# Kernel tuning notes

Measured on AMD Instinct MI355X. Metric: run time of the kernel, lower is better.

## Reference

```python
import jax, jax.numpy as jnp
import numpy as np

B, S, D, H = 4, 2048, 1024, 16
DK = D // H

def setup_inputs() -> dict:
    key = jax.random.key(0)
    ks = jax.random.split(key, 8)
    Q = jax.random.normal(ks[0], (B, S, D), dtype=jnp.float32)
    K = jax.random.normal(ks[1], (B, S, D), dtype=jnp.float32)
    V = jax.random.normal(ks[2], (B, S, D), dtype=jnp.float32)
    # causal mask: 0 means masked (as in masked_fill(mask == 0, -inf))
    mask = jnp.broadcast_to(jnp.tril(jnp.ones((S, S), dtype=jnp.int32))[None, None], (B, 1, S, S))
    scale = 1.0 / np.sqrt(D)
    W_Q = jax.random.normal(ks[3], (D, D), dtype=jnp.float32) * scale
    W_K = jax.random.normal(ks[4], (D, D), dtype=jnp.float32) * scale
    W_V = jax.random.normal(ks[5], (D, D), dtype=jnp.float32) * scale
    W_O = jax.random.normal(ks[6], (D, D), dtype=jnp.float32) * scale
    return {"Q": Q, "K": K, "V": V, "mask": mask,
            "W_Q": W_Q, "W_K": W_K, "W_V": W_V, "W_O": W_O}

def _split_heads(x):
    # [B, S, D] -> [B, H, S, DK]
    b, s, _ = x.shape
    return x.reshape(b, s, H, DK).transpose(0, 2, 1, 3)

def reference(Q, K, V, mask, W_Q, W_K, W_V, W_O):
    # nn.Linear(d,d,bias=False): y = x @ W.T ; here W_* stored as [D, D]
    q = _split_heads(Q @ W_Q.T)
    k = _split_heads(K @ W_K.T)
    v = _split_heads(V @ W_V.T)
    scores = jnp.einsum('bhqd,bhkd->bhqk', q, k) / jnp.sqrt(jnp.float32(DK))
    scores = jnp.where(mask == 0, -jnp.inf, scores)
    weights = jax.nn.softmax(scores, axis=-1)
    weights = jnp.nan_to_num(weights, nan=0.0)  # fully-masked rows -> 0
    # dropout is identity at eval / p=0
    attn = jnp.einsum('bhqk,bhkd->bhqd', weights, v)
    attn = attn.transpose(0, 2, 1, 3).reshape(Q.shape[0], Q.shape[1], D)
    return attn @ W_O.T
```

## Files before the change

### kernel.cpp

```cpp
#include <hip/hip_runtime.h>
#include <stdint.h>

#define B_  4
#define S_  2048
#define D_  1024
#define H_  16
#define DK_ 64

typedef __attribute__((ext_vector_type(8)))  short   short8;
typedef __attribute__((ext_vector_type(8)))  unsigned short ushort8;
typedef __attribute__((ext_vector_type(4)))  float   f32x4;
typedef __attribute__((ext_vector_type(16))) float   f32x16;

#define GPTR(p) ((const __attribute__((address_space(1))) void*)(p))
#define SPTR(p) ((__attribute__((address_space(3))) void*)(p))

__device__ inline unsigned short f2bf(float f) {
  uint32_t u = __float_as_uint(f);
  uint32_t r = (u + 0x7fffu + ((u >> 16) & 1u)) >> 16;
  return (unsigned short)r;
}
__device__ inline float bf2f(unsigned short h) {
  return __uint_as_float(((uint32_t)h) << 16);
}
__device__ inline uint32_t pkbf(float a, float b) {
  uint32_t r;
  asm("v_cvt_pk_bf16_f32 %0, %1, %2" : "=v"(r) : "v"(a), "v"(b));
  return r;
}
__device__ inline void pl32(uint32_t& a, uint32_t& b) {
  asm volatile("v_permlane32_swap_b32 %0, %1" : "+v"(a), "+v"(b));
}
__device__ inline short8 mk8(uint32_t a, uint32_t b, uint32_t c, uint32_t d) {
  union { uint32_t u[4]; short8 s; } x;
  x.u[0] = a; x.u[1] = b; x.u[2] = c; x.u[3] = d;
  return x.s;
}

__global__ __launch_bounds__(256) void conv_one(const float* __restrict__ src,
                                                unsigned short* __restrict__ dst,
                                                size_t n) {
  size_t i = ((size_t)blockIdx.x * blockDim.x + threadIdx.x) * 4;
  if (i < n) {
    float4 v = *reinterpret_cast<const float4*>(src + i);
    ushort4 o;
    o.x = f2bf(v.x); o.y = f2bf(v.y); o.z = f2bf(v.z); o.w = f2bf(v.w);
    *reinterpret_cast<ushort4*>(dst + i) = o;
  }
}

__global__ __launch_bounds__(256) void conv_x3(const float* __restrict__ q,
                                               const float* __restrict__ k,
                                               const float* __restrict__ v,
                                               unsigned short* __restrict__ dst) {
  const size_t NX = (size_t)B_ * S_ * D_;
  const float* src = (blockIdx.z == 0) ? q : (blockIdx.z == 1) ? k : v;
  unsigned short* d = dst + (size_t)blockIdx.z * NX;
  size_t i = ((size_t)blockIdx.x * blockDim.x + threadIdx.x) * 4;
  float4 vv = *reinterpret_cast<const float4*>(src + i);
  ushort4 o;
  o.x = f2bf(vv.x); o.y = f2bf(vv.y); o.z = f2bf(vv.z); o.w = f2bf(vv.w);
  *reinterpret_cast<ushort4*>(d + i) = o;
}

__global__ __launch_bounds__(256) void conv_w4(const float* __restrict__ w0,
                                               const float* __restrict__ w1,
                                               const float* __restrict__ w2,
                                               const float* __restrict__ w3,
                                               unsigned short* __restrict__ dst) {
  const size_t NW = (size_t)D_ * D_;
  const float* src = (blockIdx.z == 0) ? w0 : (blockIdx.z == 1) ? w1
                   : (blockIdx.z == 2) ? w2 : w3;
  unsigned short* d = dst + (size_t)blockIdx.z * NW;
  size_t i = ((size_t)blockIdx.x * blockDim.x + threadIdx.x) * 4;
  if (i < NW) {
    float4 v = *reinterpret_cast<const float4*>(src + i);
    ushort4 o;
    o.x = f2bf(v.x); o.y = f2bf(v.y); o.z = f2bf(v.z); o.w = f2bf(v.w);
    *reinterpret_cast<ushort4*>(d + i) = o;
  }
}

#define BM 128
#define BN 128
#define BK 32

__global__ __launch_bounds__(256) void gemm_qkv(const unsigned short* __restrict__ X0,
                                                const unsigned short* __restrict__ X1,
                                                const unsigned short* __restrict__ X2,
                                                const unsigned short* __restrict__ W,
                                                unsigned short* __restrict__ P,
                                                int zbase) {
  const size_t NW = (size_t)D_ * D_;
  const size_t NX = (size_t)B_ * S_ * D_;
  const int z = zbase + blockIdx.z;

  const unsigned short* A;
  const unsigned short* Bm;
  unsigned short* C;
  int N, m0, n0;
  if (z == 2) {
    A = W + 2 * NW; Bm = X2; C = P + 2 * NX;
    N = B_ * S_;
    m0 = (blockIdx.x >> 6) * BM;
    n0 = (blockIdx.x & 63) * BN;
  } else {
    A = z ? X1 : X0; Bm = W + (size_t)z * NW; C = P + (size_t)z * NX;
    N = D_;
    m0 = (blockIdx.x & 63) * BM;
    n0 = (blockIdx.x >> 6) * BN;
  }
  const int K = D_;

  __shared__ unsigned short sA[3][BM * BK];
  __shared__ unsigned short sB[3][BN * BK];

  const int tid  = threadIdx.x;
  const int lane = tid & 63;
  const int wid  = tid >> 6;
  const int wr   = wid >> 1, wc = wid & 1;
  const int g = lane >> 4, c = lane & 15;

  f32x4 acc[4][4];
#pragma unroll
  for (int m = 0; m < 4; ++m)
#pragma unroll
    for (int n = 0; n < 4; ++n) acc[m][n] = (f32x4){0.f, 0.f, 0.f, 0.f};

  auto stage = [&](int kt_, int bs) {
    const int k0 = kt_ * BK;
#pragma unroll
    for (int i = 0; i < 2; ++i) {
      const int base_ob = i * 4096 + wid * 1024;
      const int ob  = base_ob + lane * 16;
      const int row = ob >> 6;
      const int scb = (ob & 63) ^ (((ob >> 7) & 3) << 4);
      const unsigned short* ga = A  + (size_t)(m0 + row) * K + k0 + (scb >> 1);
      const unsigned short* gb = Bm + (size_t)(n0 + row) * K + k0 + (scb >> 1);
      __builtin_amdgcn_global_load_lds(GPTR(ga), SPTR(&sA[bs][base_ob >> 1]), 16, 0, 0);
      __builtin_amdgcn_global_load_lds(GPTR(gb), SPTR(&sB[bs][base_ob >> 1]), 16, 0, 0);
    }
  };

  const int nkt = K / BK;
  stage(0, 0);
  stage(1, 1);
  for (int kt = 0; kt < nkt; ++kt) {
    const int cur = kt % 3;
    if (kt + 2 < nkt) {
      stage(kt + 2, (kt + 2) % 3);
      asm volatile("s_waitcnt vmcnt(8)" ::: "memory");
    } else if (kt + 1 < nkt) {
      asm volatile("s_waitcnt vmcnt(4)" ::: "memory");
    } else {
      asm volatile("s_waitcnt vmcnt(0)" ::: "memory");
    }
    __builtin_amdgcn_sched_barrier(0);
    __builtin_amdgcn_s_barrier();
    __builtin_amdgcn_sched_barrier(0);

    short8 af[4], bf[4];
#pragma unroll
    for (int m = 0; m < 4; ++m) {
      const int ra = wr * 64 + m * 16 + c;
      af[m] = *reinterpret_cast<const short8*>(
          &sA[cur][ra * BK + ((g ^ ((ra >> 1) & 3)) << 3)]);
    }
#pragma unroll
    for (int n = 0; n < 4; ++n) {
      const int rb = wc * 64 + n * 16 + c;
      bf[n] = *reinterpret_cast<const short8*>(
          &sB[cur][rb * BK + ((g ^ ((rb >> 1) & 3)) << 3)]);
    }
    __builtin_amdgcn_s_setprio(1);
#pragma unroll
    for (int m = 0; m < 4; ++m)
#pragma unroll
      for (int n = 0; n < 4; ++n)
        acc[m][n] = __builtin_amdgcn_mfma_f32_16x16x32_bf16(af[m], bf[n], acc[m][n], 0, 0, 0);
    __builtin_amdgcn_s_setprio(0);

    asm volatile("s_waitcnt lgkmcnt(0)" ::: "memory");
    __builtin_amdgcn_sched_barrier(0);
    __builtin_amdgcn_s_barrier();
    __builtin_amdgcn_sched_barrier(0);
  }

#pragma unroll
  for (int m = 0; m < 4; ++m)
#pragma unroll
    for (int n = 0; n < 4; ++n)
#pragma unroll
      for (int r = 0; r < 4; ++r) {
        const int row = m0 + wr * 64 + m * 16 + 4 * g + r;
        const int col = n0 + wc * 64 + n * 16 + c;
        C[(size_t)row * N + col] = f2bf(acc[m][n][r]);
      }
}

__global__ __launch_bounds__(256) void gemm_out(const unsigned short* __restrict__ A,
                                                const unsigned short* __restrict__ Bm,
                                                float* __restrict__ C,
                                                int M, int N, int K) {
  __shared__ unsigned short sA[3][BM * BK];
  __shared__ unsigned short sB[3][BN * BK];

  const int tid  = threadIdx.x;
  const int lane = tid & 63;
  const int wid  = tid >> 6;
  const int wr   = wid >> 1, wc = wid & 1;
  const int g = lane >> 4, c = lane & 15;

  const int m0 = blockIdx.x * BM;
  const int n0 = blockIdx.y * BN;

  f32x4 acc[4][4];
#pragma unroll
  for (int m = 0; m < 4; ++m)
#pragma unroll
    for (int n = 0; n < 4; ++n) acc[m][n] = (f32x4){0.f, 0.f, 0.f, 0.f};

  auto stage = [&](int kt_, int bs) {
    const int k0 = kt_ * BK;
#pragma unroll
    for (int i = 0; i < 2; ++i) {
      const int base_ob = i * 4096 + wid * 1024;
      const int ob  = base_ob + lane * 16;
      const int row = ob >> 6;
      const int scb = (ob & 63) ^ (((ob >> 7) & 3) << 4);
      const unsigned short* ga = A  + (size_t)(m0 + row) * K + k0 + (scb >> 1);
      const unsigned short* gb = Bm + (size_t)(n0 + row) * K + k0 + (scb >> 1);
      __builtin_amdgcn_global_load_lds(GPTR(ga), SPTR(&sA[bs][base_ob >> 1]), 16, 0, 0);
      __builtin_amdgcn_global_load_lds(GPTR(gb), SPTR(&sB[bs][base_ob >> 1]), 16, 0, 0);
    }
  };

  const int nkt = K / BK;
  stage(0, 0);
  stage(1, 1);
  for (int kt = 0; kt < nkt; ++kt) {
    const int cur = kt % 3;
    if (kt + 2 < nkt) {
      stage(kt + 2, (kt + 2) % 3);
      asm volatile("s_waitcnt vmcnt(8)" ::: "memory");
    } else if (kt + 1 < nkt) {
      asm volatile("s_waitcnt vmcnt(4)" ::: "memory");
    } else {
      asm volatile("s_waitcnt vmcnt(0)" ::: "memory");
    }
    __builtin_amdgcn_sched_barrier(0);
    __builtin_amdgcn_s_barrier();
    __builtin_amdgcn_sched_barrier(0);

    short8 af[4], bf[4];
#pragma unroll
    for (int m = 0; m < 4; ++m) {
      const int ra = wr * 64 + m * 16 + c;
      af[m] = *reinterpret_cast<const short8*>(
          &sA[cur][ra * BK + ((g ^ ((ra >> 1) & 3)) << 3)]);
    }
#pragma unroll
    for (int n = 0; n < 4; ++n) {
      const int rb = wc * 64 + n * 16 + c;
      bf[n] = *reinterpret_cast<const short8*>(
          &sB[cur][rb * BK + ((g ^ ((rb >> 1) & 3)) << 3)]);
    }
    __builtin_amdgcn_s_setprio(1);
#pragma unroll
    for (int m = 0; m < 4; ++m)
#pragma unroll
      for (int n = 0; n < 4; ++n)
        acc[m][n] = __builtin_amdgcn_mfma_f32_16x16x32_bf16(af[m], bf[n], acc[m][n], 0, 0, 0);
    __builtin_amdgcn_s_setprio(0);

    asm volatile("s_waitcnt lgkmcnt(0)" ::: "memory");
    __builtin_amdgcn_sched_barrier(0);
    __builtin_amdgcn_s_barrier();
    __builtin_amdgcn_sched_barrier(0);
  }

#pragma unroll
  for (int m = 0; m < 4; ++m)
#pragma unroll
    for (int n = 0; n < 4; ++n)
#pragma unroll
      for (int r = 0; r < 4; ++r) {
        const int row = m0 + wr * 64 + m * 16 + 4 * g + r;
        const int col = n0 + wc * 64 + n * 16 + c;
        C[(size_t)row * N + col] = acc[m][n][r];
      }
}

__global__ __launch_bounds__(256, 4) void attn_fwd(const unsigned short* __restrict__ qp,
                                                   const unsigned short* __restrict__ kp,
                                                   const unsigned short* __restrict__ vtp,
                                                   unsigned short* __restrict__ attn) {
  const int bh = blockIdx.x;
  const int bx = blockIdx.y;
  const int b = bh >> 4, h = bh & 15;

  __shared__ unsigned short smem[4 * 64 * 64];

  const int tid  = threadIdx.x;
  const int lane = tid & 63;
  const int wid  = tid >> 6;
  const int hi   = lane >> 5;
  const int lo5  = lane & 31;

  const size_t headoff  = (size_t)b * S_ * D_ + (size_t)h * DK_;
  const size_t vheadoff = (size_t)(h * DK_) * (size_t)(B_ * S_) + (size_t)b * S_;

  const int xk = (lo5 & 7) << 4;

  auto stage = [&](int kt_, int bs) {
#pragma unroll
    for (int i = 0; i < 2; ++i) {
      const int base_ob = i * 4096 + wid * 1024;
      const int ob  = base_ob + lane * 16;
      const int row = ob >> 7;
      const int scb = (ob & 127) ^ ((row & 7) << 4);
      const unsigned short* gk = &kp[headoff + (size_t)(kt_ * 64 + row) * D_ + (scb >> 1)];
      const unsigned short* gv = &vtp[vheadoff + (size_t)row * (B_ * S_) + kt_ * 64 + (scb >> 1)];
      __builtin_amdgcn_global_load_lds(GPTR(gk), SPTR(&smem[bs * 4096 + (base_ob >> 1)]), 16, 0, 0);
      __builtin_amdgcn_global_load_lds(GPTR(gv), SPTR(&smem[8192 + bs * 4096 + (base_ob >> 1)]), 16, 0, 0);
    }
  };

#pragma unroll 1
  for (int pass = 0; pass < 2; ++pass) {
    const int qtile = pass ? bx : (15 - bx);
    const int qw = qtile * 128 + wid * 32;
    const int qg = qw + lo5;

    __syncthreads();

    short8 aq[4];
#pragma unroll
    for (int t = 0; t < 4; ++t) {
      ushort8 raw = *reinterpret_cast<const ushort8*>(
          &qp[headoff + (size_t)qg * D_ + t * 16 + hi * 8]);
      short8 sv;
#pragma unroll
      for (int j = 0; j < 8; ++j) sv[j] = (short)f2bf(bf2f(raw[j]) * 0.125f);
      aq[t] = sv;
    }

    float mrun = -3.0e38f, lrun = 0.f;
    f32x16 oa0, oa1;
#pragma unroll
    for (int r = 0; r < 16; ++r) { oa0[r] = 0.f; oa1[r] = 0.f; }

    const int nkv = 2 * (qtile + 1);
    stage(0, 0);

    for (int kt = 0; kt < nkv; ++kt) {
      const int cur = kt & 1;
      if (kt < nkv - 1) {
        stage(kt + 1, cur ^ 1);
        asm volatile("s_waitcnt vmcnt(4)" ::: "memory");
      } else {
        asm volatile("s_waitcnt vmcnt(0)" ::: "memory");
      }
      __builtin_amdgcn_sched_barrier(0);
      __builtin_amdgcn_s_barrier();
      __builtin_amdgcn_sched_barrier(0);

      const int kv0 = kt * 64;
      if (kv0 <= qw + 31) {
        const unsigned short* Kb = &smem[cur * 4096];
        const unsigned short* Vb = &smem[8192 + cur * 4096];

        f32x16 st0, st1;
#pragma unroll
        for (int r = 0; r < 16; ++r) { st0[r] = 0.f; st1[r] = 0.f; }
        __builtin_amdgcn_s_setprio(1);
#pragma unroll
        for (int t = 0; t < 4; ++t) {
          const int off = ((32 * t + 16 * hi) ^ xk) >> 1;
          short8 k0 = *reinterpret_cast<const short8*>(&Kb[lo5 * 64 + off]);
          short8 k1 = *reinterpret_cast<const short8*>(&Kb[(32 + lo5) * 64 + off]);
          st0 = __builtin_amdgcn_mfma_f32_32x32x16_bf16(k0, aq[t], st0, 0, 0, 0);
          st1 = __builtin_amdgcn_mfma_f32_32x32x16_bf16(k1, aq[t], st1, 0, 0, 0);
        }
        __builtin_amdgcn_s_setprio(0);

        if (kv0 + 63 > qw) {
#pragma unroll
          for (int r = 0; r < 16; ++r) {
            const int kvl = kv0 + (r & 3) + 8 * (r >> 2) + 4 * hi;
            if (kvl > qg)      st0[r] = -3.0e38f;
            if (kvl + 32 > qg) st1[r] = -3.0e38f;
          }
        }

        float tm = fmaxf(st0[0], st1[0]);
#pragma unroll
        for (int r = 1; r < 16; ++r) tm = fmaxf(tm, fmaxf(st0[r], st1[r]));
        tm = fmaxf(tm, __shfl_xor(tm, 32));
        const bool grow = !__all(tm <= mrun + 8.0f);
        float alpha = 1.0f;
        if (grow) {
          const float newm = fmaxf(mrun, tm);
          alpha = __expf(mrun - newm);
          mrun = newm;
        }

        float ls = 0.f;
#pragma unroll
        for (int r = 0; r < 16; ++r) { st0[r] = __expf(st0[r] - mrun); ls += st0[r]; }
        uint32_t a0 = pkbf(st0[0],  st0[1]),  a1 = pkbf(st0[2],  st0[3]);
        uint32_t b0 = pkbf(st0[4],  st0[5]),  b1 = pkbf(st0[6],  st0[7]);
        uint32_t c0 = pkbf(st0[8],  st0[9]),  c1 = pkbf(st0[10], st0[11]);
        uint32_t d0 = pkbf(st0[12], st0[13]), d1 = pkbf(st0[14], st0[15]);
        pl32(a0, b0); pl32(a1, b1);
        pl32(c0, d0); pl32(c1, d1);
        short8 pf0 = mk8(a0, a1, b0, b1);
        short8 pf1 = mk8(c0, c1, d0, d1);

#pragma unroll
        for (int r = 0; r < 16; ++r) { st1[r] = __expf(st1[r] - mrun); ls += st1[r]; }
        uint32_t e0 = pkbf(st1[0],  st1[1]),  e1 = pkbf(st1[2],  st1[3]);
        uint32_t f0 = pkbf(st1[4],  st1[5]),  f1 = pkbf(st1[6],  st1[7]);
        uint32_t g0 = pkbf(st1[8],  st1[9]),  g1 = pkbf(st1[10], st1[11]);
        uint32_t h0 = pkbf(st1[12], st1[13]), h1 = pkbf(st1[14], st1[15]);
        pl32(e0, f0); pl32(e1, f1);
        pl32(g0, h0); pl32(g1, h1);
        short8 pf2 = mk8(e0, e1, f0, f1);
        short8 pf3 = mk8(g0, g1, h0, h1);

        ls += __shfl_xor(ls, 32);
        if (grow) {
          lrun = lrun * alpha + ls;
#pragma unroll
          for (int r = 0; r < 16; ++r) { oa0[r] *= alpha; oa1[r] *= alpha; }
        } else {
          lrun += ls;
        }

        __builtin_amdgcn_s_setprio(1);
#pragma unroll
        for (int c4 = 0; c4 < 4; ++c4) {
          const int off = ((32 * c4 + 16 * hi) ^ xk) >> 1;
          short8 v0 = *reinterpret_cast<const short8*>(&Vb[lo5 * 64 + off]);
          short8 v1 = *reinterpret_cast<const short8*>(&Vb[(32 + lo5) * 64 + off]);
          const short8 pf = (c4 == 0) ? pf0 : (c4 == 1) ? pf1 : (c4 == 2) ? pf2 : pf3;
          oa0 = __builtin_amdgcn_mfma_f32_32x32x16_bf16(v0, pf, oa0, 0, 0, 0);
          oa1 = __builtin_amdgcn_mfma_f32_32x32x16_bf16(v1, pf, oa1, 0, 0, 0);
        }
        __builtin_amdgcn_s_setprio(0);
      }

      asm volatile("s_waitcnt lgkmcnt(0)" ::: "memory");
      __builtin_amdgcn_sched_barrier(0);
      __builtin_amdgcn_s_barrier();
      __builtin_amdgcn_sched_barrier(0);
    }

    {
      unsigned short* sO = &smem[wid * (32 * 72)];
      const float inv = 1.0f / lrun;
#pragma unroll
      for (int r = 0; r < 16; ++r) {
        const int dl = (r & 3) + 8 * (r >> 2) + 4 * hi;
        sO[lo5 * 72 + dl]      = f2bf(oa0[r] * inv);
        sO[lo5 * 72 + 32 + dl] = f2bf(oa1[r] * inv);
      }
      asm volatile("s_waitcnt lgkmcnt(0)" ::: "memory");
      const int row = lane >> 1, h2 = lane & 1;
      const unsigned short* src = &smem[wid * (32 * 72) + row * 72 + h2 * 32];
      unsigned short* dst = &attn[headoff + (size_t)(qtile * 128 + wid * 32 + row) * D_ + h2 * 32];
#pragma unroll
      for (int j = 0; j < 4; ++j)
        *reinterpret_cast<short8*>(dst + 8 * j) = *reinterpret_cast<const short8*>(src + 8 * j);
    }
  }
}

extern "C" void kernel_launch(void* const* d_in, const int* in_sizes, int n_in,
                              void* d_out, int out_size, void* d_ws, size_t ws_size,
                              hipStream_t stream) {
  const float* Q  = (const float*)d_in[0];
  const float* K  = (const float*)d_in[1];
  const float* V  = (const float*)d_in[2];
  const float* Wq = (const float*)d_in[4];
  const float* Wk = (const float*)d_in[5];
  const float* Wv = (const float*)d_in[6];
  const float* Wo = (const float*)d_in[7];
  float* out = (float*)d_out;

  const size_t NX = (size_t)B_ * S_ * D_;
  const size_t NW = (size_t)D_ * D_;

  const bool fused = ws_size >= 2 * (6 * NX + 4 * NW);

  unsigned short* ws = (unsigned short*)d_ws;
  unsigned short* Xq = ws;
  unsigned short* Xk = fused ? Xq + NX : Xq;
  unsigned short* Xv = fused ? Xk + NX : Xq;
  unsigned short* Wb = Xv + NX;
  unsigned short* Pj = Wb + 4 * NW;
  unsigned short* At = Xq;

  const int M = B_ * S_;
  dim3 blk(256);
  dim3 gridConvX((unsigned)(NX / 4 / 256), 1, 3);
  dim3 gridConvW((unsigned)(NW / 4 / 256), 1, 4);
  dim3 gridQKV(512, 1, 3);
  dim3 gridOut(M / BM, D_ / BN);
  dim3 gridAttn(B_ * H_, 8);

  conv_w4<<<gridConvW, blk, 0, stream>>>(Wq, Wk, Wv, Wo, Wb);

  if (fused) {
    conv_x3<<<gridConvX, blk, 0, stream>>>(Q, K, V, Xq);
    gemm_qkv<<<gridQKV, blk, 0, stream>>>(Xq, Xk, Xv, Wb, Pj, 0);
  } else {
    dim3 g1((unsigned)(NX / 4 / 256));
    dim3 gz(512, 1, 1);
    conv_one<<<g1, blk, 0, stream>>>(Q, Xq, NX);
    gemm_qkv<<<gz, blk, 0, stream>>>(Xq, Xq, Xq, Wb, Pj, 0);
    conv_one<<<g1, blk, 0, stream>>>(K, Xq, NX);
    gemm_qkv<<<gz, blk, 0, stream>>>(Xq, Xq, Xq, Wb, Pj, 1);
    conv_one<<<g1, blk, 0, stream>>>(V, Xq, NX);
    gemm_qkv<<<gz, blk, 0, stream>>>(Xq, Xq, Xq, Wb, Pj, 2);
  }

  attn_fwd<<<gridAttn, blk, 0, stream>>>(Pj, Pj + NX, Pj + 2 * NX, At);
  gemm_out<<<gridOut, blk, 0, stream>>>(At, Wb + 3 * NW, out, M, D_, D_);
}
```

Baseline: 190.9 us.

## Fuse fp32-to-bf16 activation conversion into QKV GEMM and split attention grid

The QKV projection GEMM now reads fp32 Q/K/V directly, converts them to bf16 in registers and writes the swizzled tiles to LDS, while the weights still go through direct global-to-LDS loads. This removes the separate conversion kernel and its extra round trip of activations through memory. The attention kernel drops its two-pass paired q-tile scheme and instead launches one block per q-tile (16 per head), ordering the heavy tiles first. The costs are register-staged fp32 loads with double the global bytes per tile inside the GEMM, and less balanced work per attention block.

```diff
diff --git a/kernel.cpp b/kernel.cpp
--- a/kernel.cpp
+++ b/kernel.cpp
@@ -35,32 +35,6 @@
   union { uint32_t u[4]; short8 s; } x;
   x.u[0] = a; x.u[1] = b; x.u[2] = c; x.u[3] = d;
   return x.s;
-}
-
-__global__ __launch_bounds__(256) void conv_one(const float* __restrict__ src,
-                                                unsigned short* __restrict__ dst,
-                                                size_t n) {
-  size_t i = ((size_t)blockIdx.x * blockDim.x + threadIdx.x) * 4;
-  if (i < n) {
-    float4 v = *reinterpret_cast<const float4*>(src + i);
-    ushort4 o;
-    o.x = f2bf(v.x); o.y = f2bf(v.y); o.z = f2bf(v.z); o.w = f2bf(v.w);
-    *reinterpret_cast<ushort4*>(dst + i) = o;
-  }
-}
-
-__global__ __launch_bounds__(256) void conv_x3(const float* __restrict__ q,
-                                               const float* __restrict__ k,
-                                               const float* __restrict__ v,
-                                               unsigned short* __restrict__ dst) {
-  const size_t NX = (size_t)B_ * S_ * D_;
-  const float* src = (blockIdx.z == 0) ? q : (blockIdx.z == 1) ? k : v;
-  unsigned short* d = dst + (size_t)blockIdx.z * NX;
-  size_t i = ((size_t)blockIdx.x * blockDim.x + threadIdx.x) * 4;
-  float4 vv = *reinterpret_cast<const float4*>(src + i);
-  ushort4 o;
-  o.x = f2bf(vv.x); o.y = f2bf(vv.y); o.z = f2bf(vv.z); o.w = f2bf(vv.w);
-  *reinterpret_cast<ushort4*>(d + i) = o;
 }
 
 __global__ __launch_bounds__(256) void conv_w4(const float* __restrict__ w0,
@@ -85,41 +59,158 @@
 #define BN 128
 #define BK 32
 
-__global__ __launch_bounds__(256) void gemm_qkv(const unsigned short* __restrict__ X0,
-                                                const unsigned short* __restrict__ X1,
-                                                const unsigned short* __restrict__ X2,
+__global__ __launch_bounds__(256) void gemm_qkv(const float* __restrict__ Xq,
+                                                const float* __restrict__ Xk,
+                                                const float* __restrict__ Xv,
                                                 const unsigned short* __restrict__ W,
-                                                unsigned short* __restrict__ P,
-                                                int zbase) {
+                                                unsigned short* __restrict__ P) {
   const size_t NW = (size_t)D_ * D_;
   const size_t NX = (size_t)B_ * S_ * D_;
-  const int z = zbase + blockIdx.z;
-
-  const unsigned short* A;
-  const unsigned short* Bm;
+  const int z = blockIdx.z;
+  const int K = D_;
+
+  const float* F;
   unsigned short* C;
-  int N, m0, n0;
+  int N, m0, n0, f0, h0;
   if (z == 2) {
-    A = W + 2 * NW; Bm = X2; C = P + 2 * NX;
-    N = B_ * S_;
-    m0 = (blockIdx.x >> 6) * BM;
-    n0 = (blockIdx.x & 63) * BN;
+    F = Xv; C = P + 2 * NX; N = B_ * S_;
+    n0 = (blockIdx.x & 63) * BN; f0 = n0;
+    m0 = (blockIdx.x >> 6) * BM; h0 = m0;
   } else {
-    A = z ? X1 : X0; Bm = W + (size_t)z * NW; C = P + (size_t)z * NX;
-    N = D_;
-    m0 = (blockIdx.x & 63) * BM;
-    n0 = (blockIdx.x >> 6) * BN;
-  }
-  const int K = D_;
-
-  __shared__ unsigned short sA[3][BM * BK];
-  __shared__ unsigned short sB[3][BN * BK];
+    F = z ? Xk : Xq; C = P + (size_t)z * NX; N = D_;
+    m0 = (blockIdx.x & 63) * BM; f0 = m0;
+    n0 = (blockIdx.x >> 6) * BN; h0 = n0;
+  }
+  const unsigned short* Hw = W + (size_t)z * NW;
+
+  __shared__ unsigned short sF[3][BM * BK];
+  __shared__ unsigned short sH[3][BM * BK];
 
   const int tid  = threadIdx.x;
   const int lane = tid & 63;
   const int wid  = tid >> 6;
   const int wr   = wid >> 1, wc = wid & 1;
   const int g = lane >> 4, c = lane & 15;
+  const int frow = tid >> 1, fhalf = tid & 1;
+
+  f32x4 acc[4][4];
+#pragma unroll
+  for (int m = 0; m < 4; ++m)
+#pragma unroll
+    for (int n = 0; n < 4; ++n) acc[m][n] = (f32x4){0.f, 0.f, 0.f, 0.f};
+
+  auto stageH = [&](int kt_, int bs) {
+#pragma unroll
+    for (int i = 0; i < 2; ++i) {
+      const int base_ob = i * 4096 + wid * 1024;
+      const int ob  = base_ob + lane * 16;
+      const int row = ob >> 6;
+      const int scb = (ob & 63) ^ (((ob >> 7) & 3) << 4);
+      const unsigned short* gh = Hw + (size_t)(h0 + row) * K + kt_ * BK + (scb >> 1);
+      __builtin_amdgcn_global_load_lds(GPTR(gh), SPTR(&sH[bs][base_ob >> 1]), 16, 0, 0);
+    }
+  };
+
+  float4 fA0, fA1, fA2, fA3, fB0, fB1, fB2, fB3;
+  auto loadF = [&](float4& s0, float4& s1, float4& s2, float4& s3, int kt_) {
+    const float* src_ = F + (size_t)(f0 + frow) * K + kt_ * BK + fhalf * 16;
+    s0 = *reinterpret_cast<const float4*>(src_ + 0);
+    s1 = *reinterpret_cast<const float4*>(src_ + 4);
+    s2 = *reinterpret_cast<const float4*>(src_ + 8);
+    s3 = *reinterpret_cast<const float4*>(src_ + 12);
+  };
+  auto writeF = [&](const float4& s0, const float4& s1, const float4& s2,
+                    const float4& s3, int bs) {
+    uint32_t u0 = pkbf(s0.x, s0.y), u1 = pkbf(s0.z, s0.w);
+    uint32_t u2 = pkbf(s1.x, s1.y), u3 = pkbf(s1.z, s1.w);
+    uint32_t u4 = pkbf(s2.x, s2.y), u5 = pkbf(s2.z, s2.w);
+    uint32_t u6 = pkbf(s3.x, s3.y), u7 = pkbf(s3.z, s3.w);
+    const int xr = (frow >> 1) & 3;
+    const int b0 = frow * 64 + (((fhalf * 2 + 0) ^ xr) << 4);
+    const int b1 = frow * 64 + (((fhalf * 2 + 1) ^ xr) << 4);
+    *reinterpret_cast<short8*>(&sF[bs][b0 >> 1]) = mk8(u0, u1, u2, u3);
+    *reinterpret_cast<short8*>(&sF[bs][b1 >> 1]) = mk8(u4, u5, u6, u7);
+  };
+
+  const int nkt = K / BK;
+  stageH(0, 0); loadF(fA0, fA1, fA2, fA3, 0);
+  stageH(1, 1); loadF(fB0, fB1, fB2, fB3, 1);
+  asm volatile("s_waitcnt vmcnt(6)" ::: "memory");
+  writeF(fA0, fA1, fA2, fA3, 0);
+  asm volatile("s_waitcnt lgkmcnt(0)" ::: "memory");
+  __builtin_amdgcn_sched_barrier(0);
+  __builtin_amdgcn_s_barrier();
+  __builtin_amdgcn_sched_barrier(0);
+
+  for (int kt = 0; kt < nkt; ++kt) {
+    const int cur = kt % 3;
+    const bool issue2 = (kt + 2 < nkt);
+    if (issue2) {
+      stageH(kt + 2, (kt + 2) % 3);
+      if (kt & 1) { loadF(fB0, fB1, fB2, fB3, kt + 2); }
+      else        { loadF(fA0, fA1, fA2, fA3, kt + 2); }
+    }
+
+    short8 af[4], bf[4];
+    const unsigned short* sAb = (z == 2) ? &sH[cur][0] : &sF[cur][0];
+    const unsigned short* sBb = (z == 2) ? &sF[cur][0] : &sH[cur][0];
+#pragma unroll
+    for (int m = 0; m < 4; ++m) {
+      const int ra = wr * 64 + m * 16 + c;
+      af[m] = *reinterpret_cast<const short8*>(&sAb[ra * BK + ((g ^ ((ra >> 1) & 3)) << 3)]);
+    }
+#pragma unroll
+    for (int n = 0; n < 4; ++n) {
+      const int rb = wc * 64 + n * 16 + c;
+      bf[n] = *reinterpret_cast<const short8*>(&sBb[rb * BK + ((g ^ ((rb >> 1) & 3)) << 3)]);
+    }
+    __builtin_amdgcn_s_setprio(1);
+#pragma unroll
+    for (int m = 0; m < 4; ++m)
+#pragma unroll
+      for (int n = 0; n < 4; ++n)
+        acc[m][n] = __builtin_amdgcn_mfma_f32_16x16x32_bf16(af[m], bf[n], acc[m][n], 0, 0, 0);
+    __builtin_amdgcn_s_setprio(0);
+
+    if (kt + 1 < nkt) {
+      if (issue2) { asm volatile("s_waitcnt vmcnt(6)" ::: "memory"); }
+      else        { asm volatile("s_waitcnt vmcnt(0)" ::: "memory"); }
+      if (kt & 1) { writeF(fA0, fA1, fA2, fA3, (kt + 1) % 3); }
+      else        { writeF(fB0, fB1, fB2, fB3, (kt + 1) % 3); }
+      asm volatile("s_waitcnt lgkmcnt(0)" ::: "memory");
+      __builtin_amdgcn_sched_barrier(0);
+      __builtin_amdgcn_s_barrier();
+      __builtin_amdgcn_sched_barrier(0);
+    }
+  }
+
+#pragma unroll
+  for (int m = 0; m < 4; ++m)
+#pragma unroll
+    for (int n = 0; n < 4; ++n)
+#pragma unroll
+      for (int r = 0; r < 4; ++r) {
+        const int row = m0 + wr * 64 + m * 16 + 4 * g + r;
+        const int col = n0 + wc * 64 + n * 16 + c;
+        C[(size_t)row * N + col] = f2bf(acc[m][n][r]);
+      }
+}
+
+__global__ __launch_bounds__(256) void gemm_out(const unsigned short* __restrict__ A,
+                                                const unsigned short* __restrict__ Bm,
+                                                float* __restrict__ C,
+                                                int M, int N, int K) {
+  __shared__ unsigned short sA[3][BM * BK];
+  __shared__ unsigned short sB[3][BN * BK];
+
+  const int tid  = threadIdx.x;
+  const int lane = tid & 63;
+  const int wid  = tid >> 6;
+  const int wr   = wid >> 1, wc = wid & 1;
+  const int g = lane >> 4, c = lane & 15;
+
+  const int m0 = blockIdx.x * BM;
+  const int n0 = blockIdx.y * BN;
 
   f32x4 acc[4][4];
 #pragma unroll
@@ -194,99 +285,6 @@
       for (int r = 0; r < 4; ++r) {
         const int row = m0 + wr * 64 + m * 16 + 4 * g + r;
         const int col = n0 + wc * 64 + n * 16 + c;
-        C[(size_t)row * N + col] = f2bf(acc[m][n][r]);
-      }
-}
-
-__global__ __launch_bounds__(256) void gemm_out(const unsigned short* __restrict__ A,
-                                                const unsigned short* __restrict__ Bm,
-                                                float* __restrict__ C,
-                                                int M, int N, int K) {
-  __shared__ unsigned short sA[3][BM * BK];
-  __shared__ unsigned short sB[3][BN * BK];
-
-  const int tid  = threadIdx.x;
-  const int lane = tid & 63;
-  const int wid  = tid >> 6;
-  const int wr   = wid >> 1, wc = wid & 1;
-  const int g = lane >> 4, c = lane & 15;
-
-  const int m0 = blockIdx.x * BM;
-  const int n0 = blockIdx.y * BN;
-
-  f32x4 acc[4][4];
-#pragma unroll
-  for (int m = 0; m < 4; ++m)
-#pragma unroll
-    for (int n = 0; n < 4; ++n) acc[m][n] = (f32x4){0.f, 0.f, 0.f, 0.f};
-
-  auto stage = [&](int kt_, int bs) {
-    const int k0 = kt_ * BK;
-#pragma unroll
-    for (int i = 0; i < 2; ++i) {
-      const int base_ob = i * 4096 + wid * 1024;
-      const int ob  = base_ob + lane * 16;
-      const int row = ob >> 6;
-      const int scb = (ob & 63) ^ (((ob >> 7) & 3) << 4);
-      const unsigned short* ga = A  + (size_t)(m0 + row) * K + k0 + (scb >> 1);
-      const unsigned short* gb = Bm + (size_t)(n0 + row) * K + k0 + (scb >> 1);
-      __builtin_amdgcn_global_load_lds(GPTR(ga), SPTR(&sA[bs][base_ob >> 1]), 16, 0, 0);
-      __builtin_amdgcn_global_load_lds(GPTR(gb), SPTR(&sB[bs][base_ob >> 1]), 16, 0, 0);
-    }
-  };
-
-  const int nkt = K / BK;
-  stage(0, 0);
-  stage(1, 1);
-  for (int kt = 0; kt < nkt; ++kt) {
-    const int cur = kt % 3;
-    if (kt + 2 < nkt) {
-      stage(kt + 2, (kt + 2) % 3);
-      asm volatile("s_waitcnt vmcnt(8)" ::: "memory");
-    } else if (kt + 1 < nkt) {
-      asm volatile("s_waitcnt vmcnt(4)" ::: "memory");
-    } else {
-      asm volatile("s_waitcnt vmcnt(0)" ::: "memory");
-    }
-    __builtin_amdgcn_sched_barrier(0);
-    __builtin_amdgcn_s_barrier();
-    __builtin_amdgcn_sched_barrier(0);
-
-    short8 af[4], bf[4];
-#pragma unroll
-    for (int m = 0; m < 4; ++m) {
-      const int ra = wr * 64 + m * 16 + c;
-      af[m] = *reinterpret_cast<const short8*>(
-          &sA[cur][ra * BK + ((g ^ ((ra >> 1) & 3)) << 3)]);
-    }
-#pragma unroll
-    for (int n = 0; n < 4; ++n) {
-      const int rb = wc * 64 + n * 16 + c;
-      bf[n] = *reinterpret_cast<const short8*>(
-          &sB[cur][rb * BK + ((g ^ ((rb >> 1) & 3)) << 3)]);
-    }
-    __builtin_amdgcn_s_setprio(1);
-#pragma unroll
-    for (int m = 0; m < 4; ++m)
-#pragma unroll
-      for (int n = 0; n < 4; ++n)
-        acc[m][n] = __builtin_amdgcn_mfma_f32_16x16x32_bf16(af[m], bf[n], acc[m][n], 0, 0, 0);
-    __builtin_amdgcn_s_setprio(0);
-
-    asm volatile("s_waitcnt lgkmcnt(0)" ::: "memory");
-    __builtin_amdgcn_sched_barrier(0);
-    __builtin_amdgcn_s_barrier();
-    __builtin_amdgcn_sched_barrier(0);
-  }
-
-#pragma unroll
-  for (int m = 0; m < 4; ++m)
-#pragma unroll
-    for (int n = 0; n < 4; ++n)
-#pragma unroll
-      for (int r = 0; r < 4; ++r) {
-        const int row = m0 + wr * 64 + m * 16 + 4 * g + r;
-        const int col = n0 + wc * 64 + n * 16 + c;
         C[(size_t)row * N + col] = acc[m][n][r];
       }
 }
@@ -296,7 +294,7 @@
                                                    const unsigned short* __restrict__ vtp,
                                                    unsigned short* __restrict__ attn) {
   const int bh = blockIdx.x;
-  const int bx = blockIdx.y;
+  const int qtile = 15 - (int)blockIdx.y;
   const int b = bh >> 4, h = bh & 15;
 
   __shared__ unsigned short smem[4 * 64 * 64];
@@ -326,153 +324,147 @@
     }
   };
 
-#pragma unroll 1
-  for (int pass = 0; pass < 2; ++pass) {
-    const int qtile = pass ? bx : (15 - bx);
-    const int qw = qtile * 128 + wid * 32;
-    const int qg = qw + lo5;
-
-    __syncthreads();
-
-    short8 aq[4];
-#pragma unroll
-    for (int t = 0; t < 4; ++t) {
-      ushort8 raw = *reinterpret_cast<const ushort8*>(
-          &qp[headoff + (size_t)qg * D_ + t * 16 + hi * 8]);
-      short8 sv;
-#pragma unroll
-      for (int j = 0; j < 8; ++j) sv[j] = (short)f2bf(bf2f(raw[j]) * 0.125f);
-      aq[t] = sv;
-    }
-
-    float mrun = -3.0e38f, lrun = 0.f;
-    f32x16 oa0, oa1;
-#pragma unroll
-    for (int r = 0; r < 16; ++r) { oa0[r] = 0.f; oa1[r] = 0.f; }
-
-    const int nkv = 2 * (qtile + 1);
-    stage(0, 0);
-
-    for (int kt = 0; kt < nkv; ++kt) {
-      const int cur = kt & 1;
-      if (kt < nkv - 1) {
-        stage(kt + 1, cur ^ 1);
-        asm volatile("s_waitcnt vmcnt(4)" ::: "memory");
+  const int qw = qtile * 128 + wid * 32;
+  const int qg = qw + lo5;
+
+  short8 aq[4];
+#pragma unroll
+  for (int t = 0; t < 4; ++t) {
+    ushort8 raw = *reinterpret_cast<const ushort8*>(
+        &qp[headoff + (size_t)qg * D_ + t * 16 + hi * 8]);
+    short8 sv;
+#pragma unroll
+    for (int j = 0; j < 8; ++j) sv[j] = (short)f2bf(bf2f(raw[j]) * 0.125f);
+    aq[t] = sv;
+  }
+
+  float mrun = -3.0e38f, lrun = 0.f;
+  f32x16 oa0, oa1;
+#pragma unroll
+  for (int r = 0; r < 16; ++r) { oa0[r] = 0.f; oa1[r] = 0.f; }
+
+  const int nkv = 2 * (qtile + 1);
+  stage(0, 0);
+
+  for (int kt = 0; kt < nkv; ++kt) {
+    const int cur = kt & 1;
+    if (kt < nkv - 1) {
+      stage(kt + 1, cur ^ 1);
+      asm volatile("s_waitcnt vmcnt(4)" ::: "memory");
+    } else {
+      asm volatile("s_waitcnt vmcnt(0)" ::: "memory");
+    }
+    __builtin_amdgcn_sched_barrier(0);
+    __builtin_amdgcn_s_barrier();
+    __builtin_amdgcn_sched_barrier(0);
+
+    const int kv0 = kt * 64;
+    if (kv0 <= qw + 31) {
+      const unsigned short* Kb = &smem[cur * 4096];
+      const unsigned short* Vb = &smem[8192 + cur * 4096];
+
+      f32x16 st0, st1;
+#pragma unroll
+      for (int r = 0; r < 16; ++r) { st0[r] = 0.f; st1[r] = 0.f; }
+      __builtin_amdgcn_s_setprio(1);
+#pragma unroll
+      for (int t = 0; t < 4; ++t) {
+        const int off = ((32 * t + 16 * hi) ^ xk) >> 1;
+        short8 k0 = *reinterpret_cast<const short8*>(&Kb[lo5 * 64 + off]);
+        short8 k1 = *reinterpret_cast<const short8*>(&Kb[(32 + lo5) * 64 + off]);
+        st0 = __builtin_amdgcn_mfma_f32_32x32x16_bf16(k0, aq[t], st0, 0, 0, 0);
+        st1 = __builtin_amdgcn_mfma_f32_32x32x16_bf16(k1, aq[t], st1, 0, 0, 0);
+      }
+      __builtin_amdgcn_s_setprio(0);
+
+      if (kv0 + 63 > qw) {
+#pragma unroll
+        for (int r = 0; r < 16; ++r) {
+          const int kvl = kv0 + (r & 3) + 8 * (r >> 2) + 4 * hi;
+          if (kvl > qg)      st0[r] = -3.0e38f;
+          if (kvl + 32 > qg) st1[r] = -3.0e38f;
+        }
+      }
+
+      float tm = fmaxf(st0[0], st1[0]);
+#pragma unroll
+      for (int r = 1; r < 16; ++r) tm = fmaxf(tm, fmaxf(st0[r], st1[r]));
+      tm = fmaxf(tm, __shfl_xor(tm, 32));
+      const bool grow = !__all(tm <= mrun + 8.0f);
+      float alpha = 1.0f;
+      if (grow) {
+        const float newm = fmaxf(mrun, tm);
+        alpha = __expf(mrun - newm);
+        mrun = newm;
+      }
+
+      float ls = 0.f;
+#pragma unroll
+      for (int r = 0; r < 16; ++r) { st0[r] = __expf(st0[r] - mrun); ls += st0[r]; }
+      uint32_t a0 = pkbf(st0[0],  st0[1]),  a1 = pkbf(st0[2],  st0[3]);
+      uint32_t b0 = pkbf(st0[4],  st0[5]),  b1 = pkbf(st0[6],  st0[7]);
+      uint32_t c0 = pkbf(st0[8],  st0[9]),  c1 = pkbf(st0[10], st0[11]);
+      uint32_t d0 = pkbf(st0[12], st0[13]), d1 = pkbf(st0[14], st0[15]);
+      pl32(a0, b0); pl32(a1, b1);
+      pl32(c0, d0); pl32(c1, d1);
+      short8 pf0 = mk8(a0, a1, b0, b1);
+      short8 pf1 = mk8(c0, c1, d0, d1);
+
+#pragma unroll
+      for (int r = 0; r < 16; ++r) { st1[r] = __expf(st1[r] - mrun); ls += st1[r]; }
+      uint32_t e0 = pkbf(st1[0],  st1[1]),  e1 = pkbf(st1[2],  st1[3]);
+      uint32_t f0 = pkbf(st1[4],  st1[5]),  f1 = pkbf(st1[6],  st1[7]);
+      uint32_t g0 = pkbf(st1[8],  st1[9]),  g1 = pkbf(st1[10], st1[11]);
+      uint32_t h0 = pkbf(st1[12], st1[13]), h1 = pkbf(st1[14], st1[15]);
+      pl32(e0, f0); pl32(e1, f1);
+      pl32(g0, h0); pl32(g1, h1);
+      short8 pf2 = mk8(e0, e1, f0, f1);
+      short8 pf3 = mk8(g0, g1, h0, h1);
+
+      ls += __shfl_xor(ls, 32);
+      if (grow) {
+        lrun = lrun * alpha + ls;
+#pragma unroll
+        for (int r = 0; r < 16; ++r) { oa0[r] *= alpha; oa1[r] *= alpha; }
       } else {
-        asm volatile("s_waitcnt vmcnt(0)" ::: "memory");
-      }
-      __builtin_amdgcn_sched_barrier(0);
-      __builtin_amdgcn_s_barrier();
-      __builtin_amdgcn_sched_barrier(0);
-
-      const int kv0 = kt * 64;
-      if (kv0 <= qw + 31) {
-        const unsigned short* Kb = &smem[cur * 4096];
-        const unsigned short* Vb = &smem[8192 + cur * 4096];
-
-        f32x16 st0, st1;
-#pragma unroll
-        for (int r = 0; r < 16; ++r) { st0[r] = 0.f; st1[r] = 0.f; }
-        __builtin_amdgcn_s_setprio(1);
-#pragma unroll
-        for (int t = 0; t < 4; ++t) {
-          const int off = ((32 * t + 16 * hi) ^ xk) >> 1;
-          short8 k0 = *reinterpret_cast<const short8*>(&Kb[lo5 * 64 + off]);
-          short8 k1 = *reinterpret_cast<const short8*>(&Kb[(32 + lo5) * 64 + off]);
-          st0 = __builtin_amdgcn_mfma_f32_32x32x16_bf16(k0, aq[t], st0, 0, 0, 0);
-          st1 = __builtin_amdgcn_mfma_f32_32x32x16_bf16(k1, aq[t], st1, 0, 0, 0);
-        }
-        __builtin_amdgcn_s_setprio(0);
-
-        if (kv0 + 63 > qw) {
-#pragma unroll
-          for (int r = 0; r < 16; ++r) {
-            const int kvl = kv0 + (r & 3) + 8 * (r >> 2) + 4 * hi;
-            if (kvl > qg)      st0[r] = -3.0e38f;
-            if (kvl + 32 > qg) st1[r] = -3.0e38f;
-          }
-        }
-
-        float tm = fmaxf(st0[0], st1[0]);
-#pragma unroll
-        for (int r = 1; r < 16; ++r) tm = fmaxf(tm, fmaxf(st0[r], st1[r]));
-        tm = fmaxf(tm, __shfl_xor(tm, 32));
-        const bool grow = !__all(tm <= mrun + 8.0f);
-        float alpha = 1.0f;
-        if (grow) {
-          const float newm = fmaxf(mrun, tm);
-          alpha = __expf(mrun - newm);
-          mrun = newm;
-        }
-
-        float ls = 0.f;
-#pragma unroll
-        for (int r = 0; r < 16; ++r) { st0[r] = __expf(st0[r] - mrun); ls += st0[r]; }
-        uint32_t a0 = pkbf(st0[0],  st0[1]),  a1 = pkbf(st0[2],  st0[3]);
-        uint32_t b0 = pkbf(st0[4],  st0[5]),  b1 = pkbf(st0[6],  st0[7]);
-        uint32_t c0 = pkbf(st0[8],  st0[9]),  c1 = pkbf(st0[10], st0[11]);
-        uint32_t d0 = pkbf(st0[12], st0[13]), d1 = pkbf(st0[14], st0[15]);
-        pl32(a0, b0); pl32(a1, b1);
-        pl32(c0, d0); pl32(c1, d1);
-        short8 pf0 = mk8(a0, a1, b0, b1);
-        short8 pf1 = mk8(c0, c1, d0, d1);
-
-#pragma unroll
-        for (int r = 0; r < 16; ++r) { st1[r] = __expf(st1[r] - mrun); ls += st1[r]; }
-        uint32_t e0 = pkbf(st1[0],  st1[1]),  e1 = pkbf(st1[2],  st1[3]);
-        uint32_t f0 = pkbf(st1[4],  st1[5]),  f1 = pkbf(st1[6],  st1[7]);
-        uint32_t g0 = pkbf(st1[8],  st1[9]),  g1 = pkbf(st1[10], st1[11]);
-        uint32_t h0 = pkbf(st1[12], st1[13]), h1 = pkbf(st1[14], st1[15]);
-        pl32(e0, f0); pl32(e1, f1);
-        pl32(g0, h0); pl32(g1, h1);
-        short8 pf2 = mk8(e0, e1, f0, f1);
-        short8 pf3 = mk8(g0, g1, h0, h1);
-
-        ls += __shfl_xor(ls, 32);
-        if (grow) {
-          lrun = lrun * alpha + ls;
-#pragma unroll
-          for (int r = 0; r < 16; ++r) { oa0[r] *= alpha; oa1[r] *= alpha; }
-        } else {
-          lrun += ls;
-        }
-
-        __builtin_amdgcn_s_setprio(1);
-#pragma unroll
-        for (int c4 = 0; c4 < 4; ++c4) {
-          const int off = ((32 * c4 + 16 * hi) ^ xk) >> 1;
-          short8 v0 = *reinterpret_cast<const short8*>(&Vb[lo5 * 64 + off]);
-          short8 v1 = *reinterpret_cast<const short8*>(&Vb[(32 + lo5) * 64 + off]);
-          const short8 pf = (c4 == 0) ? pf0 : (c4 == 1) ? pf1 : (c4 == 2) ? pf2 : pf3;
-          oa0 = __builtin_amdgcn_mfma_f32_32x32x16_bf16(v0, pf, oa0, 0, 0, 0);
-          oa1 = __builtin_amdgcn_mfma_f32_32x32x16_bf16(v1, pf, oa1, 0, 0, 0);
-        }
-        __builtin_amdgcn_s_setprio(0);
-      }
-
-      asm volatile("s_waitcnt lgkmcnt(0)" ::: "memory");
-      __builtin_amdgcn_sched_barrier(0);
-      __builtin_amdgcn_s_barrier();
-      __builtin_amdgcn_sched_barrier(0);
-    }
-
-    {
-      unsigned short* sO = &smem[wid * (32 * 72)];
-      const float inv = 1.0f / lrun;
-#pragma unroll
-      for (int r = 0; r < 16; ++r) {
-        const int dl = (r & 3) + 8 * (r >> 2) + 4 * hi;
-        sO[lo5 * 72 + dl]      = f2bf(oa0[r] * inv);
-        sO[lo5 * 72 + 32 + dl] = f2bf(oa1[r] * inv);
-      }
-      asm volatile("s_waitcnt lgkmcnt(0)" ::: "memory");
-      const int row = lane >> 1, h2 = lane & 1;
-      const unsigned short* src = &smem[wid * (32 * 72) + row * 72 + h2 * 32];
-      unsigned short* dst = &attn[headoff + (size_t)(qtile * 128 + wid * 32 + row) * D_ + h2 * 32];
-#pragma unroll
-      for (int j = 0; j < 4; ++j)
-        *reinterpret_cast<short8*>(dst + 8 * j) = *reinterpret_cast<const short8*>(src + 8 * j);
-    }
+        lrun += ls;
+      }
+
+      __builtin_amdgcn_s_setprio(1);
+#pragma unroll
+      for (int c4 = 0; c4 < 4; ++c4) {
+        const int off = ((32 * c4 + 16 * hi) ^ xk) >> 1;
+        short8 v0 = *reinterpret_cast<const short8*>(&Vb[lo5 * 64 + off]);
+        short8 v1 = *reinterpret_cast<const short8*>(&Vb[(32 + lo5) * 64 + off]);
+        const short8 pf = (c4 == 0) ? pf0 : (c4 == 1) ? pf1 : (c4 == 2) ? pf2 : pf3;
+        oa0 = __builtin_amdgcn_mfma_f32_32x32x16_bf16(v0, pf, oa0, 0, 0, 0);
+        oa1 = __builtin_amdgcn_mfma_f32_32x32x16_bf16(v1, pf, oa1, 0, 0, 0);
+      }
+      __builtin_amdgcn_s_setprio(0);
+    }
+
+    asm volatile("s_waitcnt lgkmcnt(0)" ::: "memory");
+    __builtin_amdgcn_sched_barrier(0);
+    __builtin_amdgcn_s_barrier();
+    __builtin_amdgcn_sched_barrier(0);
+  }
+
+  {
+    unsigned short* sO = &smem[wid * (32 * 72)];
+    const float inv = 1.0f / lrun;
+#pragma unroll
+    for (int r = 0; r < 16; ++r) {
+      const int dl = (r & 3) + 8 * (r >> 2) + 4 * hi;
+      sO[lo5 * 72 + dl]      = f2bf(oa0[r] * inv);
+      sO[lo5 * 72 + 32 + dl] = f2bf(oa1[r] * inv);
+    }
+    asm volatile("s_waitcnt lgkmcnt(0)" ::: "memory");
+    const int row = lane >> 1, h2 = lane & 1;
+    const unsigned short* src = &smem[wid * (32 * 72) + row * 72 + h2 * 32];
+    unsigned short* dst = &attn[headoff + (size_t)(qtile * 128 + wid * 32 + row) * D_ + h2 * 32];
+#pragma unroll
+    for (int j = 0; j < 4; ++j)
+      *reinterpret_cast<short8*>(dst + 8 * j) = *reinterpret_cast<const short8*>(src + 8 * j);
   }
 }
 
@@ -491,40 +483,20 @@
   const size_t NX = (size_t)B_ * S_ * D_;
   const size_t NW = (size_t)D_ * D_;
 
-  const bool fused = ws_size >= 2 * (6 * NX + 4 * NW);
-
   unsigned short* ws = (unsigned short*)d_ws;
-  unsigned short* Xq = ws;
-  unsigned short* Xk = fused ? Xq + NX : Xq;
-  unsigned short* Xv = fused ? Xk + NX : Xq;
-  unsigned short* Wb = Xv + NX;
+  unsigned short* Wb = ws;
   unsigned short* Pj = Wb + 4 * NW;
-  unsigned short* At = Xq;
+  unsigned short* At = Pj + 3 * NX;
 
   const int M = B_ * S_;
   dim3 blk(256);
-  dim3 gridConvX((unsigned)(NX / 4 / 256), 1, 3);
   dim3 gridConvW((unsigned)(NW / 4 / 256), 1, 4);
   dim3 gridQKV(512, 1, 3);
   dim3 gridOut(M / BM, D_ / BN);
-  dim3 gridAttn(B_ * H_, 8);
+  dim3 gridAttn(B_ * H_, 16);
 
   conv_w4<<<gridConvW, blk, 0, stream>>>(Wq, Wk, Wv, Wo, Wb);
-
-  if (fused) {
-    conv_x3<<<gridConvX, blk, 0, stream>>>(Q, K, V, Xq);
-    gemm_qkv<<<gridQKV, blk, 0, stream>>>(Xq, Xk, Xv, Wb, Pj, 0);
-  } else {
-    dim3 g1((unsigned)(NX / 4 / 256));
-    dim3 gz(512, 1, 1);
-    conv_one<<<g1, blk, 0, stream>>>(Q, Xq, NX);
-    gemm_qkv<<<gz, blk, 0, stream>>>(Xq, Xq, Xq, Wb, Pj, 0);
-    conv_one<<<g1, blk, 0, stream>>>(K, Xq, NX);
-    gemm_qkv<<<gz, blk, 0, stream>>>(Xq, Xq, Xq, Wb, Pj, 1);
-    conv_one<<<g1, blk, 0, stream>>>(V, Xq, NX);
-    gemm_qkv<<<gz, blk, 0, stream>>>(Xq, Xq, Xq, Wb, Pj, 2);
-  }
-
+  gemm_qkv<<<gridQKV, blk, 0, stream>>>(Q, K, V, Wb, Pj);
   attn_fwd<<<gridAttn, blk, 0, stream>>>(Pj, Pj + NX, Pj + 2 * NX, At);
   gemm_out<<<gridOut, blk, 0, stream>>>(At, Wb + 3 * NW, out, M, D_, D_);
 }
```

New measurement: 211.1 us. 1.11x slower.
